# Kernel optimization log

Hardware: AMD Instinct MI355X
Metric: run time of the kernel (lower is better)

Reference implementation:

```python
import jax, jax.numpy as jnp
import numpy as np

N_NODES = 100000


def _gcn_conv(x, W, b, src, dst, n):
    # PyG GCNConv: h = x @ W; add self-loops; norm = d^-1/2[src] * d^-1/2[dst];
    # out[i] = sum_{(s->i)} norm * h[s] + b
    h = x @ W  # [N, F_out]
    deg = jax.ops.segment_sum(jnp.ones_like(dst, dtype=h.dtype), dst, num_segments=n)
    dis = jnp.where(deg > 0, jax.lax.rsqrt(jnp.maximum(deg, 1.0)), 0.0)
    norm = dis[src] * dis[dst]  # [E]
    msg = h[src] * norm[:, None]  # [E, F_out] gather + scale
    out = jax.ops.segment_sum(msg, dst, num_segments=n)  # scatter-add
    return out + b


def _add_self_loops(edge_index, n):
    loops = jnp.arange(n, dtype=edge_index.dtype)
    src = jnp.concatenate([edge_index[0], loops])
    dst = jnp.concatenate([edge_index[1], loops])
    return src, dst


def setup_inputs() -> dict:
    key = jax.random.key(0)
    k_x, k_e, k_w1, k_w2 = jax.random.split(key, 4)
    n, e, f_in, f_hid = N_NODES, 1600000, 128, 64
    x = jax.random.normal(k_x, (n, f_in), dtype=jnp.float32)
    edge_index = jax.random.randint(k_e, (2, e), 0, n, dtype=jnp.int64)
    # Glorot-ish init for weights
    W1 = jax.random.normal(k_w1, (f_in, f_hid), dtype=jnp.float32) / np.sqrt(f_in)
    b1 = jnp.zeros((f_hid,), dtype=jnp.float32)
    W2 = jax.random.normal(k_w2, (f_hid, f_hid), dtype=jnp.float32) / np.sqrt(f_hid)
    b2 = jnp.zeros((f_hid,), dtype=jnp.float32)
    return {"x": x, "edge_index": edge_index, "W1": W1, "b1": b1, "W2": W2, "b2": b2}


def reference(x, edge_index, W1, b1, W2, b2):
    n = x.shape[0]
    src, dst = _add_self_loops(edge_index, n)
    h = jax.nn.relu(_gcn_conv(x, W1, b1, src, dst, n))
    # F.dropout(training=False) in eval mode is identity
    out = _gcn_conv(h, W2, b2, src, dst, n)
    return out
```

## Files before the change

kernel.cpp:

```cpp
#include <hip/hip_runtime.h>
#include <hip/hip_bf16.h>


#define FOUT 64
#define BW 256
#define BSH 8
#define MAXB 512
#define CHUNK 4096
#define SLAB 6144

#define NT1 1024
#define NT2 512

__device__ __forceinline__ float bf2f(unsigned int u16) {
    union { unsigned int i; float f; } c;
    c.i = u16 << 16;
    return c.f;
}
__device__ __forceinline__ unsigned short f2bf(float f) {
    union { float f; unsigned int i; } c;
    c.f = f;
    unsigned int i = c.i;
    return (unsigned short)((i + 0x7FFFu + ((i >> 16) & 1u)) >> 16);
}

typedef __attribute__((ext_vector_type(8))) short short8v;
typedef __attribute__((ext_vector_type(4))) float f32x4;

__device__ __forceinline__ void conv_w_frag(const float* __restrict__ W,
                                            unsigned short* __restrict__ WhF,
                                            unsigned short* __restrict__ WlF,
                                            int task) {
    const int lane = task & 63;
    const int cf = (task >> 6) & 3;
    const int s = task >> 8;
    const int q = lane >> 4, m = lane & 15;
#pragma unroll
    for (int j = 0; j < 8; j++) {
        int k = s * 32 + q * 8 + j;
        float x = W[(size_t)k * 64 + cf * 16 + m];
        unsigned short h = f2bf(x);
        WhF[(size_t)task * 8 + j] = h;
        WlF[(size_t)task * 8 + j] = f2bf(x - bf2f(h));
    }
}

__global__ __launch_bounds__(512) void edge_hist(
    const int* __restrict__ dst, int* __restrict__ cnt, int E,
    const float* __restrict__ W1, const float* __restrict__ W2,
    unsigned short* __restrict__ whf1, unsigned short* __restrict__ wlf1,
    unsigned short* __restrict__ whf2, unsigned short* __restrict__ wlf2) {
    __shared__ int h[MAXB];
    const int blk = blockIdx.x, t = threadIdx.x;
    h[t] = 0;
    __syncthreads();
    const int e0 = blk * CHUNK;
#pragma unroll
    for (int k = 0; k < CHUNK / 512; k++) {
        int e = e0 + k * 512 + t;
        if (e < E) atomicAdd(&h[dst[e] >> BSH], 1);
    }
    if (blk == 0) {
        for (int task = t; task < NT1 + NT2; task += 512) {
            if (task < NT1) conv_w_frag(W1, whf1, wlf1, task);
            else            conv_w_frag(W2, whf2, wlf2, task - NT1);
        }
    }
    __syncthreads();
    cnt[blk * MAXB + t] = h[t];
}

__global__ __launch_bounds__(512) void col_scan(int* __restrict__ cnt, int nblk,
                                                int* __restrict__ gcnt) {
    __shared__ int ts[512];
    const int b = blockIdx.x;
    const int t = threadIdx.x;
    int v = (t < nblk) ? cnt[t * MAXB + b] : 0;
    ts[t] = v;
    __syncthreads();
    for (int off = 1; off < 512; off <<= 1) {
        int x = (t >= off) ? ts[t - off] : 0;
        __syncthreads();
        ts[t] += x;
        __syncthreads();
    }
    if (t < nblk) cnt[t * MAXB + b] = b * SLAB + ts[t] - v;
    if (t == 511) gcnt[b] = ts[511];
}

__global__ __launch_bounds__(512) void edge_place(
    const int* __restrict__ src, const int* __restrict__ dst,
    const int* __restrict__ cnt, int* __restrict__ ebuf, int E) {
    __shared__ int lbase[MAXB];
    __shared__ int cur[MAXB];
    const int blk = blockIdx.x, t = threadIdx.x;
    lbase[t] = cnt[blk * MAXB + t];
    cur[t] = 0;
    __syncthreads();
    const int e0 = blk * CHUNK;
#pragma unroll
    for (int k = 0; k < CHUNK / 512; k++) {
        int e = e0 + k * 512 + t;
        if (e < E) {
            int d = dst[e];
            int b = d >> BSH;
            int r = atomicAdd(&cur[b], 1);
            ebuf[lbase[b] + r] = src[e] | ((d & (BW - 1)) << 17);
        }
    }
}

__global__ __launch_bounds__(512) void csr_build(
    int* __restrict__ ebuf, const int* __restrict__ gcnt,
    unsigned int* __restrict__ rowinfo, float* __restrict__ dis, int n) {
    __shared__ int ldeg[BW];
    __shared__ int lscan[BW];
    const int b = blockIdx.x, t = threadIdx.x;
    const int node0 = b << BSH;
    const int nn = min(BW, n - node0);
    const int ebeg = b * SLAB;
    const int cnt = gcnt[b];

    int w[SLAB / 512];
#pragma unroll
    for (int k = 0; k < SLAB / 512; k++) {
        int idx = t + k * 512;
        w[k] = (idx < cnt) ? ebuf[ebeg + idx] : -1;
    }
    if (t < BW) ldeg[t] = 0;
    __syncthreads();
#pragma unroll
    for (int k = 0; k < SLAB / 512; k++)
        if (w[k] >= 0) atomicAdd(&ldeg[w[k] >> 17], 1);
    __syncthreads();
    int v = 0;
    if (t < BW) {
        v = ldeg[t];
        lscan[t] = v;
    }
    __syncthreads();
    for (int off = 1; off < BW; off <<= 1) {
        int x = 0;
        if (t < BW && t >= off) x = lscan[t - off];
        __syncthreads();
        if (t < BW) lscan[t] += x;
        __syncthreads();
    }
    if (t < nn) {
        int ex = lscan[t] - v;
        rowinfo[node0 + t] = ((unsigned int)(ebeg + ex) << 8) | (unsigned int)v;
        dis[node0 + t] = rsqrtf((float)v + 1.0f);
    }
    __syncthreads();
    if (t < BW) ldeg[t] = lscan[t] - v;
    __syncthreads();
#pragma unroll
    for (int k = 0; k < SLAB / 512; k++)
        if (w[k] >= 0) {
            int r = atomicAdd(&ldeg[w[k] >> 17], 1);
            ebuf[ebeg + r] = w[k] & 0x1FFFF;
        }
}

template <int K>
__global__ __launch_bounds__(256) void gemm_xw_mfma(
    const float* __restrict__ X,
    const unsigned short* __restrict__ WhF,
    const unsigned short* __restrict__ WlF,
    const float* __restrict__ dis,
    unsigned short* __restrict__ HS, int n) {
    const int lane = threadIdx.x & 63;
    const int wv = threadIdx.x >> 6;
    const int wrow0 = blockIdx.x * 64 + wv * 16;
    const int m = lane & 15;
    const int q = lane >> 4;

    f32x4 acc[4];
#pragma unroll
    for (int cf = 0; cf < 4; cf++) acc[cf] = (f32x4)0.f;

    const int arow = wrow0 + m;
    const bool rok = (arow < n);
    const float* xp = X + (size_t)arow * K + q * 8;

#pragma unroll
    for (int s = 0; s < K / 32; s++) {
        float4 v0, v1;
        if (rok) {
            v0 = *(const float4*)(xp + s * 32);
            v1 = *(const float4*)(xp + s * 32 + 4);
        } else {
            v0 = make_float4(0.f, 0.f, 0.f, 0.f);
            v1 = v0;
        }
        const float xa[8] = {v0.x, v0.y, v0.z, v0.w, v1.x, v1.y, v1.z, v1.w};
        union { unsigned int u[4]; short8v v; } Ah, Al;
#pragma unroll
        for (int p = 0; p < 4; p++) {
            unsigned short h0 = f2bf(xa[2 * p]);
            unsigned short h1 = f2bf(xa[2 * p + 1]);
            Ah.u[p] = (unsigned int)h0 | ((unsigned int)h1 << 16);
            unsigned short l0 = f2bf(xa[2 * p] - bf2f(h0));
            unsigned short l1 = f2bf(xa[2 * p + 1] - bf2f(h1));
            Al.u[p] = (unsigned int)l0 | ((unsigned int)l1 << 16);
        }
        const unsigned short* wh = WhF + ((size_t)(s * 4) * 64 + lane) * 8;
        const unsigned short* wl = WlF + ((size_t)(s * 4) * 64 + lane) * 8;
#pragma unroll
        for (int cf = 0; cf < 4; cf++) {
            short8v bh = *(const short8v*)(wh + (size_t)cf * 64 * 8);
            short8v bl = *(const short8v*)(wl + (size_t)cf * 64 * 8);
            acc[cf] = __builtin_amdgcn_mfma_f32_16x16x32_bf16(Ah.v, bh, acc[cf], 0, 0, 0);
            acc[cf] = __builtin_amdgcn_mfma_f32_16x16x32_bf16(Al.v, bh, acc[cf], 0, 0, 0);
            acc[cf] = __builtin_amdgcn_mfma_f32_16x16x32_bf16(Ah.v, bl, acc[cf], 0, 0, 0);
        }
    }
#pragma unroll
    for (int r = 0; r < 4; r++) {
        int row = wrow0 + q * 4 + r;
        if (row < n) {
            float dr = dis[row];
#pragma unroll
            for (int cf = 0; cf < 4; cf++) {
                HS[(size_t)row * FOUT + cf * 16 + m] = f2bf(acc[cf][r] * dr);
            }
        }
    }
}

__device__ __forceinline__ void acc8(const uint4 u, float* a) {
    a[0] += bf2f(u.x & 0xFFFFu); a[1] += bf2f(u.x >> 16);
    a[2] += bf2f(u.y & 0xFFFFu); a[3] += bf2f(u.y >> 16);
    a[4] += bf2f(u.z & 0xFFFFu); a[5] += bf2f(u.z >> 16);
    a[6] += bf2f(u.w & 0xFFFFu); a[7] += bf2f(u.w >> 16);
}

template <bool RELU>
__global__ __launch_bounds__(256) void aggregate(
    const uint4* __restrict__ hsv, const unsigned int* __restrict__ rowinfo,
    const int* __restrict__ col, const float* __restrict__ dis,
    const float* __restrict__ bias, float* __restrict__ out, int n) {
    const int wave = blockIdx.x * 4 + (threadIdx.x >> 6);
    const int lane = threadIdx.x & 63;
    const int g  = lane >> 3;
    const int jj = lane & 7;
    const int i = wave * 8 + g;
    if (i >= n) return;

    const unsigned int info = rowinfo[i];
    const int beg = (int)(info >> 8);
    const int end = beg + (int)(info & 255u);

    float a[8];
    acc8(hsv[(size_t)i * 8 + jj], a);
    {
        uint4 su = hsv[(size_t)i * 8 + jj];
        a[0] = bf2f(su.x & 0xFFFFu); a[1] = bf2f(su.x >> 16);
        a[2] = bf2f(su.y & 0xFFFFu); a[3] = bf2f(su.y >> 16);
        a[4] = bf2f(su.z & 0xFFFFu); a[5] = bf2f(su.z >> 16);
        a[6] = bf2f(su.w & 0xFFFFu); a[7] = bf2f(su.w >> 16);
    }

    const int gb = g << 3;
    for (int chunk = beg; chunk < end; chunk += 8) {
        int m = end - chunk;
        if (m > 8) m = 8;
        int c = (chunk + jj < end) ? col[chunk + jj] : 0;
        int q = 0;
        for (; q + 4 <= m; q += 4) {
            int s0 = __shfl(c, gb + q);
            int s1 = __shfl(c, gb + q + 1);
            int s2 = __shfl(c, gb + q + 2);
            int s3 = __shfl(c, gb + q + 3);
            uint4 u0 = hsv[(size_t)s0 * 8 + jj];
            uint4 u1 = hsv[(size_t)s1 * 8 + jj];
            uint4 u2 = hsv[(size_t)s2 * 8 + jj];
            uint4 u3 = hsv[(size_t)s3 * 8 + jj];
            acc8(u0, a);
            acc8(u1, a);
            acc8(u2, a);
            acc8(u3, a);
        }
        for (; q < m; q++) {
            int s = __shfl(c, gb + q);
            acc8(hsv[(size_t)s * 8 + jj], a);
        }
    }
    float d = dis[i];
    const float4* b4 = (const float4*)bias;
    float4 bb0 = b4[jj * 2];
    float4 bb1 = b4[jj * 2 + 1];
    float4 o0, o1;
    o0.x = d * a[0] + bb0.x; o0.y = d * a[1] + bb0.y;
    o0.z = d * a[2] + bb0.z; o0.w = d * a[3] + bb0.w;
    o1.x = d * a[4] + bb1.x; o1.y = d * a[5] + bb1.y;
    o1.z = d * a[6] + bb1.z; o1.w = d * a[7] + bb1.w;
    if (RELU) {
        o0.x = fmaxf(o0.x, 0.f); o0.y = fmaxf(o0.y, 0.f);
        o0.z = fmaxf(o0.z, 0.f); o0.w = fmaxf(o0.w, 0.f);
        o1.x = fmaxf(o1.x, 0.f); o1.y = fmaxf(o1.y, 0.f);
        o1.z = fmaxf(o1.z, 0.f); o1.w = fmaxf(o1.w, 0.f);
    }
    float4* orow = (float4*)out + (size_t)i * 16 + jj * 2;
    orow[0] = o0;
    orow[1] = o1;
}

extern "C" void kernel_launch(void* const* d_in, const int* in_sizes, int n_in,
                              void* d_out, int out_size, void* d_ws, size_t ws_size,
                              hipStream_t stream) {
    const float* x  = (const float*)d_in[0];
    const int*   ei = (const int*)d_in[1];
    const float* W1 = (const float*)d_in[2];
    const float* b1 = (const float*)d_in[3];
    const float* W2 = (const float*)d_in[4];
    const float* b2 = (const float*)d_in[5];

    const int n = in_sizes[0] / 128;
    const int E = in_sizes[1] / 2;
    const int* srcp = ei;
    const int* dstp = ei + E;

    float* out = (float*)d_out;

    const int B = (n + BW - 1) / BW;
    const int nblk = (E + CHUNK - 1) / CHUNK;

    int*            cnt     = (int*)d_ws;
    int*            gcnt    = cnt + 512 * MAXB;
    unsigned int*   rowinfo = (unsigned int*)(gcnt + MAXB);
    float*          dis     = (float*)(rowinfo + n);
    int*            ebuf    = (int*)(dis + n);
    unsigned short* hs      = (unsigned short*)(ebuf + (size_t)B * SLAB);
    unsigned short* whf1    = hs + (size_t)n * FOUT;
    unsigned short* wlf1    = whf1 + (size_t)NT1 * 8;
    unsigned short* whf2    = wlf1 + (size_t)NT1 * 8;
    unsigned short* wlf2    = whf2 + (size_t)NT2 * 8;

    edge_hist<<<nblk, 512, 0, stream>>>(dstp, cnt, E, W1, W2,
                                        whf1, wlf1, whf2, wlf2);
    col_scan<<<B, 512, 0, stream>>>(cnt, nblk, gcnt);
    edge_place<<<nblk, 512, 0, stream>>>(srcp, dstp, cnt, ebuf, E);
    csr_build<<<B, 512, 0, stream>>>(ebuf, gcnt, rowinfo, dis, n);

    gemm_xw_mfma<128><<<(n + 63) / 64, 256, 0, stream>>>(x, whf1, wlf1, dis, hs, n);
    aggregate<true><<<(n + 31) / 32, 256, 0, stream>>>(
        (const uint4*)hs, rowinfo, ebuf, dis, b1, out, n);

    gemm_xw_mfma<64><<<(n + 63) / 64, 256, 0, stream>>>(out, whf2, wlf2, dis, hs, n);
    aggregate<false><<<(n + 31) / 32, 256, 0, stream>>>(
        (const uint4*)hs, rowinfo, ebuf, dis, b2, out, n);
}
```

Baseline: 229.9 us.

## Fuse CSR build with layer-1 GEMM and layer-1 aggregation with layer-2 GEMM

Merges the CSR build kernel with the first X·W1 MFMA GEMM, so each block computes its 256 nodes' degree normalisation into shared memory and then projects those rows. It also fuses the first aggregation (with bias and ReLU) with the second GEMM: the aggregated 32x64 tile is staged in LDS and multiplied by W2, so the fp32 hidden activations never go to global memory. Two launches and a full N×64 fp32 round trip are removed. The cost is heavier fused kernels: 512-thread CSR blocks now also carry GEMM work, and the aggregation kernel adds an LDS tile and a barrier. A separate hs2 buffer is added, and a stray duplicate acc8 call on uninitialised accumulators is removed.

New measurement: 224.0 us. 2.6% less time.

```diff
diff --git a/kernel.cpp b/kernel.cpp
--- a/kernel.cpp
+++ b/kernel.cpp
@@ -26,6 +26,21 @@
 
 typedef __attribute__((ext_vector_type(8))) short short8v;
 typedef __attribute__((ext_vector_type(4))) float f32x4;
+
+__device__ __forceinline__ void split_frag(const float* xa, short8v* Ah, short8v* Al) {
+    union { unsigned int u[4]; short8v v; } H, L;
+#pragma unroll
+    for (int p = 0; p < 4; p++) {
+        unsigned short h0 = f2bf(xa[2 * p]);
+        unsigned short h1 = f2bf(xa[2 * p + 1]);
+        H.u[p] = (unsigned int)h0 | ((unsigned int)h1 << 16);
+        unsigned short l0 = f2bf(xa[2 * p] - bf2f(h0));
+        unsigned short l1 = f2bf(xa[2 * p + 1] - bf2f(h1));
+        L.u[p] = (unsigned int)l0 | ((unsigned int)l1 << 16);
+    }
+    *Ah = H.v;
+    *Al = L.v;
+}
 
 __device__ __forceinline__ void conv_w_frag(const float* __restrict__ W,
                                             unsigned short* __restrict__ WhF,
@@ -110,11 +125,15 @@
     }
 }
 
-__global__ __launch_bounds__(512) void csr_build(
+template <int K>
+__global__ __launch_bounds__(512) void csr_gemm(
     int* __restrict__ ebuf, const int* __restrict__ gcnt,
-    unsigned int* __restrict__ rowinfo, float* __restrict__ dis, int n) {
+    unsigned int* __restrict__ rowinfo, float* __restrict__ dis, int n,
+    const float* __restrict__ X, const unsigned short* __restrict__ WhF,
+    const unsigned short* __restrict__ WlF, unsigned short* __restrict__ HS) {
     __shared__ int ldeg[BW];
     __shared__ int lscan[BW];
+    __shared__ float sdis[BW];
     const int b = blockIdx.x, t = threadIdx.x;
     const int node0 = b << BSH;
     const int nn = min(BW, n - node0);
@@ -149,7 +168,11 @@
     if (t < nn) {
         int ex = lscan[t] - v;
         rowinfo[node0 + t] = ((unsigned int)(ebeg + ex) << 8) | (unsigned int)v;
-        dis[node0 + t] = rsqrtf((float)v + 1.0f);
+        float dv = rsqrtf((float)v + 1.0f);
+        dis[node0 + t] = dv;
+        sdis[t] = dv;
+    } else if (t < BW) {
+        sdis[t] = 0.f;
     }
     __syncthreads();
     if (t < BW) ldeg[t] = lscan[t] - v;
@@ -160,69 +183,55 @@
             int r = atomicAdd(&ldeg[w[k] >> 17], 1);
             ebuf[ebeg + r] = w[k] & 0x1FFFF;
         }
-}
-
-template <int K>
-__global__ __launch_bounds__(256) void gemm_xw_mfma(
-    const float* __restrict__ X,
-    const unsigned short* __restrict__ WhF,
-    const unsigned short* __restrict__ WlF,
-    const float* __restrict__ dis,
-    unsigned short* __restrict__ HS, int n) {
-    const int lane = threadIdx.x & 63;
-    const int wv = threadIdx.x >> 6;
-    const int wrow0 = blockIdx.x * 64 + wv * 16;
+
+    const int lane = t & 63;
+    const int wvv = t >> 6;
     const int m = lane & 15;
     const int q = lane >> 4;
-
-    f32x4 acc[4];
-#pragma unroll
-    for (int cf = 0; cf < 4; cf++) acc[cf] = (f32x4)0.f;
-
-    const int arow = wrow0 + m;
-    const bool rok = (arow < n);
-    const float* xp = X + (size_t)arow * K + q * 8;
-
-#pragma unroll
-    for (int s = 0; s < K / 32; s++) {
-        float4 v0, v1;
-        if (rok) {
-            v0 = *(const float4*)(xp + s * 32);
-            v1 = *(const float4*)(xp + s * 32 + 4);
-        } else {
-            v0 = make_float4(0.f, 0.f, 0.f, 0.f);
-            v1 = v0;
-        }
-        const float xa[8] = {v0.x, v0.y, v0.z, v0.w, v1.x, v1.y, v1.z, v1.w};
-        union { unsigned int u[4]; short8v v; } Ah, Al;
-#pragma unroll
-        for (int p = 0; p < 4; p++) {
-            unsigned short h0 = f2bf(xa[2 * p]);
-            unsigned short h1 = f2bf(xa[2 * p + 1]);
-            Ah.u[p] = (unsigned int)h0 | ((unsigned int)h1 << 16);
-            unsigned short l0 = f2bf(xa[2 * p] - bf2f(h0));
-            unsigned short l1 = f2bf(xa[2 * p + 1] - bf2f(h1));
-            Al.u[p] = (unsigned int)l0 | ((unsigned int)l1 << 16);
-        }
-        const unsigned short* wh = WhF + ((size_t)(s * 4) * 64 + lane) * 8;
-        const unsigned short* wl = WlF + ((size_t)(s * 4) * 64 + lane) * 8;
-#pragma unroll
-        for (int cf = 0; cf < 4; cf++) {
-            short8v bh = *(const short8v*)(wh + (size_t)cf * 64 * 8);
-            short8v bl = *(const short8v*)(wl + (size_t)cf * 64 * 8);
-            acc[cf] = __builtin_amdgcn_mfma_f32_16x16x32_bf16(Ah.v, bh, acc[cf], 0, 0, 0);
-            acc[cf] = __builtin_amdgcn_mfma_f32_16x16x32_bf16(Al.v, bh, acc[cf], 0, 0, 0);
-            acc[cf] = __builtin_amdgcn_mfma_f32_16x16x32_bf16(Ah.v, bl, acc[cf], 0, 0, 0);
-        }
-    }
-#pragma unroll
-    for (int r = 0; r < 4; r++) {
-        int row = wrow0 + q * 4 + r;
-        if (row < n) {
-            float dr = dis[row];
+#pragma unroll 1
+    for (int t2 = 0; t2 < 2; t2++) {
+        const int tile = wvv * 2 + t2;
+        const int wrow0 = node0 + tile * 16;
+        f32x4 acc[4];
+#pragma unroll
+        for (int cf = 0; cf < 4; cf++) acc[cf] = (f32x4)0.f;
+
+        const int arow = wrow0 + m;
+        const bool rok = (arow < n);
+        const float* xp = X + (size_t)arow * K + q * 8;
+#pragma unroll
+        for (int s = 0; s < K / 32; s++) {
+            float4 v0, v1;
+            if (rok) {
+                v0 = *(const float4*)(xp + s * 32);
+                v1 = *(const float4*)(xp + s * 32 + 4);
+            } else {
+                v0 = make_float4(0.f, 0.f, 0.f, 0.f);
+                v1 = v0;
+            }
+            const float xa[8] = {v0.x, v0.y, v0.z, v0.w, v1.x, v1.y, v1.z, v1.w};
+            short8v Ah, Al;
+            split_frag(xa, &Ah, &Al);
+            const unsigned short* wh = WhF + ((size_t)(s * 4) * 64 + lane) * 8;
+            const unsigned short* wl = WlF + ((size_t)(s * 4) * 64 + lane) * 8;
 #pragma unroll
             for (int cf = 0; cf < 4; cf++) {
-                HS[(size_t)row * FOUT + cf * 16 + m] = f2bf(acc[cf][r] * dr);
+                short8v bh = *(const short8v*)(wh + (size_t)cf * 64 * 8);
+                short8v bl = *(const short8v*)(wl + (size_t)cf * 64 * 8);
+                acc[cf] = __builtin_amdgcn_mfma_f32_16x16x32_bf16(Ah, bh, acc[cf], 0, 0, 0);
+                acc[cf] = __builtin_amdgcn_mfma_f32_16x16x32_bf16(Al, bh, acc[cf], 0, 0, 0);
+                acc[cf] = __builtin_amdgcn_mfma_f32_16x16x32_bf16(Ah, bl, acc[cf], 0, 0, 0);
+            }
+        }
+#pragma unroll
+        for (int r = 0; r < 4; r++) {
+            int row = wrow0 + q * 4 + r;
+            if (row < n) {
+                float dr = sdis[tile * 16 + q * 4 + r];
+#pragma unroll
+                for (int cf = 0; cf < 4; cf++) {
+                    HS[(size_t)row * FOUT + cf * 16 + m] = f2bf(acc[cf][r] * dr);
+                }
             }
         }
     }
@@ -233,6 +242,125 @@
     a[2] += bf2f(u.y & 0xFFFFu); a[3] += bf2f(u.y >> 16);
     a[4] += bf2f(u.z & 0xFFFFu); a[5] += bf2f(u.z >> 16);
     a[6] += bf2f(u.w & 0xFFFFu); a[7] += bf2f(u.w >> 16);
+}
+
+#define OSTR 68
+__global__ __launch_bounds__(256) void agg_gemm(
+    const uint4* __restrict__ hsv, const unsigned int* __restrict__ rowinfo,
+    const int* __restrict__ col, const float* __restrict__ dis,
+    const float* __restrict__ bias,
+    const unsigned short* __restrict__ WhF2, const unsigned short* __restrict__ WlF2,
+    unsigned short* __restrict__ HS2, int n) {
+    __shared__ float so[32 * OSTR];
+    const int tid = threadIdx.x;
+    const int wv = tid >> 6;
+    const int lane = tid & 63;
+    const int g = lane >> 3;
+    const int jj = lane & 7;
+    const int lrow = wv * 8 + g;
+    const int i = blockIdx.x * 32 + lrow;
+
+    float o[8];
+#pragma unroll
+    for (int p = 0; p < 8; p++) o[p] = 0.f;
+
+    if (i < n) {
+        const unsigned int info = rowinfo[i];
+        const int beg = (int)(info >> 8);
+        const int end = beg + (int)(info & 255u);
+
+        float a[8];
+        {
+            uint4 su = hsv[(size_t)i * 8 + jj];
+            a[0] = bf2f(su.x & 0xFFFFu); a[1] = bf2f(su.x >> 16);
+            a[2] = bf2f(su.y & 0xFFFFu); a[3] = bf2f(su.y >> 16);
+            a[4] = bf2f(su.z & 0xFFFFu); a[5] = bf2f(su.z >> 16);
+            a[6] = bf2f(su.w & 0xFFFFu); a[7] = bf2f(su.w >> 16);
+        }
+        const int gb = g << 3;
+        for (int chunk = beg; chunk < end; chunk += 8) {
+            int m = end - chunk;
+            if (m > 8) m = 8;
+            int c = (chunk + jj < end) ? col[chunk + jj] : 0;
+            int q = 0;
+            for (; q + 4 <= m; q += 4) {
+                int s0 = __shfl(c, gb + q);
+                int s1 = __shfl(c, gb + q + 1);
+                int s2 = __shfl(c, gb + q + 2);
+                int s3 = __shfl(c, gb + q + 3);
+                uint4 u0 = hsv[(size_t)s0 * 8 + jj];
+                uint4 u1 = hsv[(size_t)s1 * 8 + jj];
+                uint4 u2 = hsv[(size_t)s2 * 8 + jj];
+                uint4 u3 = hsv[(size_t)s3 * 8 + jj];
+                acc8(u0, a);
+                acc8(u1, a);
+                acc8(u2, a);
+                acc8(u3, a);
+            }
+            for (; q < m; q++) {
+                int s = __shfl(c, gb + q);
+                acc8(hsv[(size_t)s * 8 + jj], a);
+            }
+        }
+        float d = dis[i];
+        const float4* b4 = (const float4*)bias;
+        float4 bb0 = b4[jj * 2];
+        float4 bb1 = b4[jj * 2 + 1];
+        o[0] = fmaxf(d * a[0] + bb0.x, 0.f);
+        o[1] = fmaxf(d * a[1] + bb0.y, 0.f);
+        o[2] = fmaxf(d * a[2] + bb0.z, 0.f);
+        o[3] = fmaxf(d * a[3] + bb0.w, 0.f);
+        o[4] = fmaxf(d * a[4] + bb1.x, 0.f);
+        o[5] = fmaxf(d * a[5] + bb1.y, 0.f);
+        o[6] = fmaxf(d * a[6] + bb1.z, 0.f);
+        o[7] = fmaxf(d * a[7] + bb1.w, 0.f);
+    }
+    {
+        float* sp = &so[lrow * OSTR + jj * 8];
+        *(float4*)sp = make_float4(o[0], o[1], o[2], o[3]);
+        *(float4*)(sp + 4) = make_float4(o[4], o[5], o[6], o[7]);
+    }
+    __syncthreads();
+
+    const int tile = wv >> 1;
+    const int ch = wv & 1;
+    const int m = lane & 15;
+    const int q = lane >> 4;
+    f32x4 acc[2];
+    acc[0] = (f32x4)0.f;
+    acc[1] = (f32x4)0.f;
+#pragma unroll
+    for (int s = 0; s < 2; s++) {
+        const float* ap = &so[(tile * 16 + m) * OSTR + s * 32 + q * 8];
+        float4 v0 = *(const float4*)ap;
+        float4 v1 = *(const float4*)(ap + 4);
+        const float xa[8] = {v0.x, v0.y, v0.z, v0.w, v1.x, v1.y, v1.z, v1.w};
+        short8v Ah, Al;
+        split_frag(xa, &Ah, &Al);
+#pragma unroll
+        for (int c = 0; c < 2; c++) {
+            int cf = ch * 2 + c;
+            const unsigned short* wh = WhF2 + ((size_t)(s * 4 + cf) * 64 + lane) * 8;
+            const unsigned short* wl = WlF2 + ((size_t)(s * 4 + cf) * 64 + lane) * 8;
+            short8v bh = *(const short8v*)wh;
+            short8v bl = *(const short8v*)wl;
+            acc[c] = __builtin_amdgcn_mfma_f32_16x16x32_bf16(Ah, bh, acc[c], 0, 0, 0);
+            acc[c] = __builtin_amdgcn_mfma_f32_16x16x32_bf16(Al, bh, acc[c], 0, 0, 0);
+            acc[c] = __builtin_amdgcn_mfma_f32_16x16x32_bf16(Ah, bl, acc[c], 0, 0, 0);
+        }
+    }
+#pragma unroll
+    for (int r = 0; r < 4; r++) {
+        int lr = tile * 16 + q * 4 + r;
+        int i2 = blockIdx.x * 32 + lr;
+        if (i2 < n) {
+            float dr = dis[i2];
+#pragma unroll
+            for (int c = 0; c < 2; c++) {
+                HS2[(size_t)i2 * FOUT + (ch * 2 + c) * 16 + m] = f2bf(acc[c][r] * dr);
+            }
+        }
+    }
 }
 
 template <bool RELU>
@@ -252,7 +380,6 @@
     const int end = beg + (int)(info & 255u);
 
     float a[8];
-    acc8(hsv[(size_t)i * 8 + jj], a);
     {
         uint4 su = hsv[(size_t)i * 8 + jj];
         a[0] = bf2f(su.x & 0xFFFFu); a[1] = bf2f(su.x >> 16);
@@ -336,18 +463,19 @@
     unsigned short* wlf1    = whf1 + (size_t)NT1 * 8;
     unsigned short* whf2    = wlf1 + (size_t)NT1 * 8;
     unsigned short* wlf2    = whf2 + (size_t)NT2 * 8;
+    unsigned short* hs2     = wlf2 + (size_t)NT2 * 8;
 
     edge_hist<<<nblk, 512, 0, stream>>>(dstp, cnt, E, W1, W2,
                                         whf1, wlf1, whf2, wlf2);
     col_scan<<<B, 512, 0, stream>>>(cnt, nblk, gcnt);
     edge_place<<<nblk, 512, 0, stream>>>(srcp, dstp, cnt, ebuf, E);
-    csr_build<<<B, 512, 0, stream>>>(ebuf, gcnt, rowinfo, dis, n);
-
-    gemm_xw_mfma<128><<<(n + 63) / 64, 256, 0, stream>>>(x, whf1, wlf1, dis, hs, n);
-    aggregate<true><<<(n + 31) / 32, 256, 0, stream>>>(
-        (const uint4*)hs, rowinfo, ebuf, dis, b1, out, n);
-
-    gemm_xw_mfma<64><<<(n + 63) / 64, 256, 0, stream>>>(out, whf2, wlf2, dis, hs, n);
+
+    csr_gemm<128><<<B, 512, 0, stream>>>(ebuf, gcnt, rowinfo, dis, n,
+                                         x, whf1, wlf1, hs);
+
+    agg_gemm<<<(n + 31) / 32, 256, 0, stream>>>(
+        (const uint4*)hs, rowinfo, ebuf, dis, b1, whf2, wlf2, hs2, n);
+
     aggregate<false><<<(n + 31) / 32, 256, 0, stream>>>(
-        (const uint4*)hs, rowinfo, ebuf, dis, b2, out, n);
-}
+        (const uint4*)hs2, rowinfo, ebuf, dis, b2, out, n);
+}
```
